# Kernel tuning notes

Measured on AMD Instinct MI355X. Metric: run time of the kernel, lower is better.

The kernel has to match this reference:

```python
import math
import jax, jax.numpy as jnp
import numpy as np

# ---- module constants (from init_kwargs) ----
B, IN, OUT, NR = 4096, 512, 512, 16
WL_MIN, WL_MAX = 1546.0e-9, 1554.0e-9
WL0 = 0.5 * (WL_MIN + WL_MAX)          # center wavelength
R_UM, NEFF, NG = 30.0, 2.34, 4.2
LOSS_DB_CM, KAPPA = 3.0, 0.2
L = 2.0 * math.pi * (R_UM * 1e-6)      # ring circumference [m]
A_AMP = 10.0 ** (-LOSS_DB_CM * (L * 100.0) / 20.0)  # single-pass amplitude
R_T = math.sqrt(1.0 - KAPPA)           # through-coupling amplitude


def _ring_neffs():
    # per-ring effective index detuning from phase_offsets (as in __init__)
    offsets = jnp.linspace(-math.pi, math.pi, NR, dtype=jnp.float32)
    return jnp.float32(NEFF) + offsets * jnp.float32(WL0 / (2.0 * math.pi * L))  # [NR]


def _evaluate_basis(x):
    # wavelengths driven by (clamped) inputs: [B, IN]
    wl = WL_MIN + 0.5 * (jnp.clip(x, -1.0, 1.0) + 1.0) * (WL_MAX - WL_MIN)
    wl = wl[..., None]                                  # [B, IN, 1]
    neff_r = _ring_neffs()                              # [NR]
    # first-order dispersion around WL0 (waveguide with neff, ng)
    neff_wl = neff_r - (wl - WL0) * (NG - neff_r) / WL0  # [B, IN, NR]
    phi = (2.0 * math.pi * L) * neff_wl / wl            # round-trip phase
    c = jnp.cos(phi)
    # all-pass ring power throughput (analytic transfer function)
    num = A_AMP * A_AMP - 2.0 * R_T * A_AMP * c + R_T * R_T
    den = 1.0 - 2.0 * R_T * A_AMP * c + (R_T * A_AMP) ** 2
    return num / den                                    # [B, IN, NR]


def setup_inputs() -> dict:
    key = jax.random.key(0)
    k1, k2, k3 = jax.random.split(key, 3)
    x = jax.random.normal(k1, (B, IN), dtype=jnp.float32)
    coeffs = jax.random.normal(k2, (IN, OUT, NR), dtype=jnp.float32) * 0.05
    base_weight = jax.random.normal(k3, (IN, OUT), dtype=jnp.float32) * 0.05
    return {"x": x, "coeffs": coeffs, "base_weight": base_weight}


def reference(x, coeffs, base_weight):
    basis = _evaluate_basis(x)                          # [B, IN, NR]
    basis_out = jnp.einsum('bin,ion->bo', basis, coeffs)  # [B, OUT]
    residual = x @ base_weight                          # [B, OUT]
    kl = jnp.zeros((1,), dtype=x.dtype)                 # non-variational path
    return (basis_out + residual, kl)
```

## Files before the change

### kernel.cpp

```cpp
#include <hip/hip_runtime.h>
#include <hip/hip_bf16.h>
#include <cmath>
#include <cstdint>

#define Bsz   4096
#define INsz  512
#define OUTsz 512
#define NRING 16
#define KTOT  8704
#define SPLITK 8
#define NPH   17

using short8 = __attribute__((ext_vector_type(8))) short;
using f32x4  = __attribute__((ext_vector_type(4))) float;

struct RC {
  float Cr[NRING];
  float Snr[NRING];
  float K2, SQ, pad0, pad1;
};

__device__ __forceinline__ unsigned short f2bf(float f) {
  __hip_bfloat16 h = __float2bfloat16(f);
  return *reinterpret_cast<unsigned short*>(&h);
}
__device__ __forceinline__ float bf2f(unsigned short u) {
  union { unsigned int u; float f; } v; v.u = (unsigned int)u << 16;
  return v.f;
}
__device__ __forceinline__ float fastrcp(float x) {
#if __has_builtin(__builtin_amdgcn_rcpf)
  return __builtin_amdgcn_rcpf(x);
#else
  return 1.0f / x;
#endif
}
__device__ __forceinline__ float fastfract(float x) {
#if __has_builtin(__builtin_amdgcn_fractf)
  return __builtin_amdgcn_fractf(x);
#else
  return x - floorf(x);
#endif
}
__device__ __forceinline__ float cos2pi(float fr) {
#if __has_builtin(__builtin_amdgcn_cosf)
  return __builtin_amdgcn_cosf(fr);
#else
  return __cosf(fr * 6.28318530717958647692f);
#endif
}
__device__ __forceinline__ float sin2pi(float fr) {
#if __has_builtin(__builtin_amdgcn_sinf)
  return __builtin_amdgcn_sinf(fr);
#else
  return __sinf(fr * 6.28318530717958647692f);
#endif
}

__device__ __forceinline__ void gl_lds16(const void* g, void* l) {
  __builtin_amdgcn_global_load_lds(
      (const __attribute__((address_space(1))) void*)g,
      (__attribute__((address_space(3))) void*)l, 16, 0, 0);
}

__global__ __launch_bounds__(512) void pack_b_kernel(
    const float* __restrict__ coeffs, const float* __restrict__ bw,
    unsigned short* __restrict__ Bt, float* __restrict__ bias, float PQ) {
  __shared__ float red[8];
  const int o = blockIdx.x;
  const int i = threadIdx.x;
  const float* cp = coeffs + ((size_t)i * OUTsz + o) * NRING;
  unsigned short* row = Bt + (size_t)o * KTOT + i;
  float s = 0.0f;
#pragma unroll
  for (int j = 0; j < 4; ++j) {
    f32x4 v = *reinterpret_cast<const f32x4*>(cp + j * 4);
#pragma unroll
    for (int e = 0; e < 4; ++e) {
      const int n = j * 4 + e;
      s += v[e];
      row[(size_t)n * INsz] = f2bf(PQ * v[e]);
    }
  }
  row[(size_t)NRING * INsz] = f2bf(bw[(size_t)i * OUTsz + o]);
#pragma unroll
  for (int off = 32; off > 0; off >>= 1) s += __shfl_down(s, off);
  const int w = i >> 6;
  if ((i & 63) == 0) red[w] = s;
  __syncthreads();
  if (i == 0) {
    float t = 0.0f;
#pragma unroll
    for (int k = 0; k < 8; ++k) t += red[k];
    bias[o] = t;
  }
}

__global__ __launch_bounds__(512, 4) void gemm_fused_kernel(
    const float* __restrict__ x, const unsigned short* __restrict__ Bt,
    unsigned short* __restrict__ part, RC rc) {
  extern __shared__ char smem[];
  char* smA = smem;
  char* smB = smem + 32768;
  const int tid  = threadIdx.x;
  const int lane = tid & 63;
  const int w    = tid >> 6;
  const int bid  = blockIdx.x;
  const int combo = bid & 31;
  const int rb   = bid >> 5;
  const int cb   = combo & 3, ks = combo >> 2;
  const int brow = rb * 128, bcol = cb * 128;

  const int r  = tid & 127;
  const int q4 = tid >> 7;
  const int wb0 = r * 128 + (((q4 * 2 + 0) ^ (r & 7)) * 16);
  const int wb1 = r * 128 + (((q4 * 2 + 1) ^ (r & 7)) * 16);

  const int cg = (lane & 7) ^ ((lane >> 3) & 7);
  const unsigned short* gb0 = Bt + (size_t)(bcol + w * 8 + (lane >> 3)) * KTOT
                                 + ks * 64 + cg * 8;

  const int wr = w >> 2, wc = w & 3;
  const int l7 = lane & 7;
  const int rowA = wr * 64 + (lane & 15);
  const int rowB = wc * 32 + (lane & 15);

  float cth[16], sth[16];
  short8 xbfa, xbfb;
  {
    float xf[16];
    const float* gx = x + (size_t)(brow + r) * INsz + ks * 64 + q4 * 16;
#pragma unroll
    for (int j = 0; j < 4; ++j) {
      f32x4 v = *reinterpret_cast<const f32x4*>(gx + j * 4);
#pragma unroll
      for (int e = 0; e < 4; ++e) xf[j * 4 + e] = v[e];
    }
#pragma unroll
    for (int c = 0; c < 8; ++c) {
      xbfa[c] = (short)f2bf(xf[c]);
      xbfb[c] = (short)f2bf(xf[c + 8]);
    }
#pragma unroll
    for (int c = 0; c < 16; ++c) {
      float xc = fminf(fmaxf(xf[c], -1.0f), 1.0f);
      float wl = __builtin_fmaf(xc, 4.0e-9f, 1550.0e-9f);
      float hh = rc.K2 * xc * fastrcp(wl);
      float fr = fastfract(hh);
      cth[c] = cos2pi(fr);
      sth[c] = sin2pi(fr);
    }
  }

  auto STAGE = [&](int p) {
    char* ldst = smB + (p % 3) * 16384 + w * 1024;
    const unsigned short* src = gb0 + (size_t)p * 512;
    gl_lds16(src, ldst);
    gl_lds16(src + (size_t)64 * KTOT, ldst + 8192);
  };
  auto GENA = [&](int p) {
    char* dst = smA + (p & 1) * 16384;
    if (p < NRING) {
      const float Crn = rc.Cr[p], Snn = rc.Snr[p];
#pragma unroll
      for (int g = 0; g < 2; ++g) {
        short8 wv;
#pragma unroll
        for (int e = 0; e < 8; ++e) {
          float cph = __builtin_fmaf(cth[g * 8 + e], Crn, sth[g * 8 + e] * Snn);
          wv[e] = (short)f2bf(fastrcp(cph + rc.SQ));
        }
        *reinterpret_cast<short8*>(dst + (g ? wb1 : wb0)) = wv;
      }
    } else {
      *reinterpret_cast<short8*>(dst + wb0) = xbfa;
      *reinterpret_cast<short8*>(dst + wb1) = xbfb;
    }
  };

  f32x4 acc[4][2];
#pragma unroll
  for (int m = 0; m < 4; ++m)
#pragma unroll
    for (int q = 0; q < 2; ++q) acc[m][q] = (f32x4){0.f, 0.f, 0.f, 0.f};

  STAGE(0); STAGE(1);
  GENA(0);
  asm volatile("s_waitcnt vmcnt(2) lgkmcnt(0)" ::: "memory");
  __builtin_amdgcn_s_barrier();
  __builtin_amdgcn_sched_barrier(0);

#pragma unroll
  for (int p = 0; p < NPH; ++p) {
    if (p + 2 < NPH) STAGE(p + 2);
    if (p + 1 < NPH) GENA(p + 1);
    const char* bA = smA + (p & 1) * 16384;
    const char* bB = smB + (p % 3) * 16384;
#pragma unroll
    for (int kk = 0; kk < 2; ++kk) {
      const int oct = (((lane >> 4) + kk * 4) ^ l7) * 16;
      short8 af[4], bfr[2];
#pragma unroll
      for (int m = 0; m < 4; ++m)
        af[m] = *reinterpret_cast<const short8*>(bA + (rowA + m * 16) * 128 + oct);
#pragma unroll
      for (int q = 0; q < 2; ++q)
        bfr[q] = *reinterpret_cast<const short8*>(bB + (rowB + q * 16) * 128 + oct);
      __builtin_amdgcn_s_setprio(1);
#pragma unroll
      for (int m = 0; m < 4; ++m)
#pragma unroll
        for (int q = 0; q < 2; ++q)
          acc[m][q] = __builtin_amdgcn_mfma_f32_16x16x32_bf16(af[m], bfr[q], acc[m][q], 0, 0, 0);
      __builtin_amdgcn_s_setprio(0);
    }
    if (p + 1 < NPH) {
      if (p + 2 < NPH) {
        asm volatile("s_waitcnt vmcnt(2) lgkmcnt(0)" ::: "memory");
      } else {
        asm volatile("s_waitcnt vmcnt(0) lgkmcnt(0)" ::: "memory");
      }
      __builtin_amdgcn_s_barrier();
      __builtin_amdgcn_sched_barrier(0);
    }
  }

  unsigned short* po = part + (size_t)ks * ((size_t)Bsz * OUTsz);
  const int r0 = brow + wr * 64 + ((lane >> 4) * 4);
  const int c0 = bcol + wc * 32 + (lane & 15);
#pragma unroll
  for (int m = 0; m < 4; ++m)
#pragma unroll
    for (int q = 0; q < 2; ++q)
#pragma unroll
      for (int e = 0; e < 4; ++e)
        po[(size_t)(r0 + m * 16 + e) * OUTsz + (c0 + q * 16)] = f2bf(acc[m][q][e]);
}

__global__ __launch_bounds__(256) void reduce_kernel(
    const unsigned short* __restrict__ part, const float* __restrict__ bias,
    float* __restrict__ out) {
  const size_t idx  = (size_t)blockIdx.x * 256 + threadIdx.x;
  const size_t base = idx * 8;
  float s[8];
#pragma unroll
  for (int e = 0; e < 8; ++e) s[e] = 0.0f;
#pragma unroll
  for (int sp = 0; sp < SPLITK; ++sp) {
    short8 v = *reinterpret_cast<const short8*>(part + sp * ((size_t)Bsz * OUTsz) + base);
#pragma unroll
    for (int e = 0; e < 8; ++e) s[e] += bf2f((unsigned short)v[e]);
  }
  const int ob = (int)(base & (OUTsz - 1));
  f32x4 b0 = *reinterpret_cast<const f32x4*>(bias + ob);
  f32x4 b1 = *reinterpret_cast<const f32x4*>(bias + ob + 4);
  f32x4 o0 = { s[0] + b0[0], s[1] + b0[1], s[2] + b0[2], s[3] + b0[3] };
  f32x4 o1 = { s[4] + b1[0], s[5] + b1[1], s[6] + b1[2], s[7] + b1[3] };
  *reinterpret_cast<f32x4*>(out + base) = o0;
  *reinterpret_cast<f32x4*>(out + base + 4) = o1;
  if (idx == 0) out[(size_t)Bsz * OUTsz] = 0.0f;
}

extern "C" void kernel_launch(void* const* d_in, const int* in_sizes, int n_in,
                              void* d_out, int out_size, void* d_ws, size_t ws_size,
                              hipStream_t stream) {
  const float* x      = (const float*)d_in[0];
  const float* coeffs = (const float*)d_in[1];
  const float* bw     = (const float*)d_in[2];
  float* out = (float*)d_out;

  unsigned short* Bt   = (unsigned short*)d_ws;
  unsigned short* part = (unsigned short*)((char*)d_ws + (size_t)OUTsz * KTOT * 2);
  float* bias = (float*)((char*)d_ws + (size_t)OUTsz * KTOT * 2
                                     + (size_t)SPLITK * Bsz * OUTsz * 2);

  RC rc;
  float PQ;
  {
    const double PI  = 3.14159265358979323846;
    const double Lc  = 2.0 * PI * 30.0e-6;
    const double WL0 = 1550.0e-9;
    const double NG  = 4.2;
    const double Aamp = pow(10.0, -3.0 * (Lc * 100.0) / 20.0);
    const double Rt2  = 0.8;
    const double Rt   = sqrt(Rt2);
    for (int rr = 0; rr < NRING; ++rr) {
      double off  = -PI + rr * (2.0 * PI / 15.0);
      double neff = 2.34 + off * WL0 / (2.0 * PI * Lc);
      double rev0 = (Lc / WL0) * neff;
      rc.Cr[rr]  = (float)cos(2.0 * PI * rev0);
      rc.Snr[rr] = (float)(-sin(2.0 * PI * rev0));
    }
    const double qn = -2.0 * Rt * Aamp;
    const double s  = 1.0 + Rt2 * Aamp * Aamp;
    const double P  = -(1.0 - Aamp * Aamp) * (1.0 - Rt2);
    rc.K2 = (float)(-4.0e-9 * Lc * NG / WL0);
    rc.SQ = (float)(s / qn);
    rc.pad0 = rc.pad1 = 0.f;
    PQ = (float)(P / qn);
  }

  hipFuncSetAttribute(reinterpret_cast<const void*>(gemm_fused_kernel),
                      hipFuncAttributeMaxDynamicSharedMemorySize, 81920);

  hipLaunchKernelGGL(pack_b_kernel, dim3(OUTsz), dim3(512), 0, stream,
                     coeffs, bw, Bt, bias, PQ);
  hipLaunchKernelGGL(gemm_fused_kernel, dim3(1024), dim3(512), 81920, stream,
                     x, Bt, part, rc);
  hipLaunchKernelGGL(reduce_kernel, dim3((Bsz * OUTsz / 8) / 256), dim3(256), 0, stream,
                     part, bias, out);
}
```

Before: 68.88 us.

## Enlarge GEMM tiles to 256x256, single-buffer A, compute ring phase via fract+cos

Each block now computes a 256x256 output tile instead of 128x128, cutting the grid from 1024 to 256 blocks and raising per-wave MFMA work (8x4 accumulators). The goal is more operand reuse per LDS load and less global B traffic. The A basis tile is now single-buffered. It is regenerated between two barriers each phase, after the second half's fragments are already in registers. The ring phase is now computed as a per-ring fractional offset added to the input phase, followed by one cos, instead of a cos/sin rotation. This drops the sin evaluation and the precomputed sin/cos arrays. The trade-offs are lower occupancy, one block per CU with higher register pressure, and less latency hiding for the basis generation.

```diff
diff --git a/kernel.cpp b/kernel.cpp
--- a/kernel.cpp
+++ b/kernel.cpp
@@ -15,8 +15,7 @@
 using f32x4  = __attribute__((ext_vector_type(4))) float;
 
 struct RC {
-  float Cr[NRING];
-  float Snr[NRING];
+  float Fr[NRING];
   float K2, SQ, pad0, pad1;
 };
 
@@ -47,13 +46,6 @@
   return __builtin_amdgcn_cosf(fr);
 #else
   return __cosf(fr * 6.28318530717958647692f);
-#endif
-}
-__device__ __forceinline__ float sin2pi(float fr) {
-#if __has_builtin(__builtin_amdgcn_sinf)
-  return __builtin_amdgcn_sinf(fr);
-#else
-  return __sinf(fr * 6.28318530717958647692f);
 #endif
 }
 
@@ -96,7 +88,7 @@
   }
 }
 
-__global__ __launch_bounds__(512, 4) void gemm_fused_kernel(
+__global__ __launch_bounds__(512, 2) void gemm_fused_kernel(
     const float* __restrict__ x, const unsigned short* __restrict__ Bt,
     unsigned short* __restrict__ part, RC rc) {
   extern __shared__ char smem[];
@@ -106,15 +98,18 @@
   const int lane = tid & 63;
   const int w    = tid >> 6;
   const int bid  = blockIdx.x;
-  const int combo = bid & 31;
-  const int rb   = bid >> 5;
-  const int cb   = combo & 3, ks = combo >> 2;
-  const int brow = rb * 128, bcol = cb * 128;
-
-  const int r  = tid & 127;
-  const int q4 = tid >> 7;
-  const int wb0 = r * 128 + (((q4 * 2 + 0) ^ (r & 7)) * 16);
-  const int wb1 = r * 128 + (((q4 * 2 + 1) ^ (r & 7)) * 16);
+  const int combo = bid & 15;
+  const int rb   = bid >> 4;
+  const int cb   = combo & 1, ks = combo >> 1;
+  const int brow = rb * 256, bcol = cb * 256;
+
+  const int r  = tid & 255;
+  const int h  = tid >> 8;
+  int wb[4];
+#pragma unroll
+  for (int g = 0; g < 4; ++g)
+    wb[g] = r * 128 + (((h * 4 + g) ^ (r & 7)) * 16);
+  const float* gx = x + (size_t)(brow + r) * INsz + ks * 64 + h * 32;
 
   const int cg = (lane & 7) ^ ((lane >> 3) & 7);
   const unsigned short* gb0 = Bt + (size_t)(bcol + w * 8 + (lane >> 3)) * KTOT
@@ -122,101 +117,110 @@
 
   const int wr = w >> 2, wc = w & 3;
   const int l7 = lane & 7;
-  const int rowA = wr * 64 + (lane & 15);
-  const int rowB = wc * 32 + (lane & 15);
-
-  float cth[16], sth[16];
-  short8 xbfa, xbfb;
-  {
-    float xf[16];
-    const float* gx = x + (size_t)(brow + r) * INsz + ks * 64 + q4 * 16;
-#pragma unroll
-    for (int j = 0; j < 4; ++j) {
-      f32x4 v = *reinterpret_cast<const f32x4*>(gx + j * 4);
-#pragma unroll
-      for (int e = 0; e < 4; ++e) xf[j * 4 + e] = v[e];
-    }
-#pragma unroll
-    for (int c = 0; c < 8; ++c) {
-      xbfa[c] = (short)f2bf(xf[c]);
-      xbfb[c] = (short)f2bf(xf[c + 8]);
-    }
-#pragma unroll
-    for (int c = 0; c < 16; ++c) {
-      float xc = fminf(fmaxf(xf[c], -1.0f), 1.0f);
+  const int rowA = wr * 128 + (lane & 15);
+  const int rowB = wc * 64 + (lane & 15);
+  const int oct0 = (((lane >> 4) + 0) ^ l7) * 16;
+  const int oct1 = (((lane >> 4) + 4) ^ l7) * 16;
+
+  float hrev[32];
+#pragma unroll
+  for (int j = 0; j < 8; ++j) {
+    f32x4 v = *reinterpret_cast<const f32x4*>(gx + j * 4);
+#pragma unroll
+    for (int e = 0; e < 4; ++e) {
+      float xc = fminf(fmaxf(v[e], -1.0f), 1.0f);
       float wl = __builtin_fmaf(xc, 4.0e-9f, 1550.0e-9f);
-      float hh = rc.K2 * xc * fastrcp(wl);
-      float fr = fastfract(hh);
-      cth[c] = cos2pi(fr);
-      sth[c] = sin2pi(fr);
+      hrev[j * 4 + e] = rc.K2 * xc * fastrcp(wl);
     }
   }
 
   auto STAGE = [&](int p) {
-    char* ldst = smB + (p % 3) * 16384 + w * 1024;
+    char* ldst = smB + (p % 3) * 32768 + w * 1024;
     const unsigned short* src = gb0 + (size_t)p * 512;
-    gl_lds16(src, ldst);
-    gl_lds16(src + (size_t)64 * KTOT, ldst + 8192);
+#pragma unroll
+    for (int iss = 0; iss < 4; ++iss)
+      gl_lds16(src + (size_t)iss * 64 * KTOT, ldst + iss * 8192);
   };
-  auto GENA = [&](int p) {
-    char* dst = smA + (p & 1) * 16384;
-    if (p < NRING) {
-      const float Crn = rc.Cr[p], Snn = rc.Snr[p];
-#pragma unroll
-      for (int g = 0; g < 2; ++g) {
+  auto GENA = [&](int ring) {
+    if (ring < NRING) {
+      const float Frn = rc.Fr[ring];
+#pragma unroll
+      for (int g = 0; g < 4; ++g) {
         short8 wv;
 #pragma unroll
         for (int e = 0; e < 8; ++e) {
-          float cph = __builtin_fmaf(cth[g * 8 + e], Crn, sth[g * 8 + e] * Snn);
+          float t = fastfract(hrev[g * 8 + e] + Frn);
+          float cph = cos2pi(t);
           wv[e] = (short)f2bf(fastrcp(cph + rc.SQ));
         }
-        *reinterpret_cast<short8*>(dst + (g ? wb1 : wb0)) = wv;
+        *reinterpret_cast<short8*>(smA + wb[g]) = wv;
       }
     } else {
-      *reinterpret_cast<short8*>(dst + wb0) = xbfa;
-      *reinterpret_cast<short8*>(dst + wb1) = xbfb;
+#pragma unroll
+      for (int g = 0; g < 4; ++g) {
+        f32x4 v0 = *reinterpret_cast<const f32x4*>(gx + g * 8);
+        f32x4 v1 = *reinterpret_cast<const f32x4*>(gx + g * 8 + 4);
+        short8 wv;
+#pragma unroll
+        for (int e = 0; e < 4; ++e) {
+          wv[e]     = (short)f2bf(v0[e]);
+          wv[4 + e] = (short)f2bf(v1[e]);
+        }
+        *reinterpret_cast<short8*>(smA + wb[g]) = wv;
+      }
     }
   };
 
-  f32x4 acc[4][2];
-#pragma unroll
-  for (int m = 0; m < 4; ++m)
-#pragma unroll
-    for (int q = 0; q < 2; ++q) acc[m][q] = (f32x4){0.f, 0.f, 0.f, 0.f};
+  f32x4 acc[8][4];
+#pragma unroll
+  for (int m = 0; m < 8; ++m)
+#pragma unroll
+    for (int q = 0; q < 4; ++q) acc[m][q] = (f32x4){0.f, 0.f, 0.f, 0.f};
 
   STAGE(0); STAGE(1);
   GENA(0);
-  asm volatile("s_waitcnt vmcnt(2) lgkmcnt(0)" ::: "memory");
+  asm volatile("s_waitcnt vmcnt(4) lgkmcnt(0)" ::: "memory");
   __builtin_amdgcn_s_barrier();
   __builtin_amdgcn_sched_barrier(0);
 
 #pragma unroll
   for (int p = 0; p < NPH; ++p) {
+    const char* bB = smB + (p % 3) * 32768;
+    short8 af[8], bv[4];
+#pragma unroll
+    for (int m = 0; m < 8; ++m)
+      af[m] = *reinterpret_cast<const short8*>(smA + (rowA + m * 16) * 128 + oct0);
+#pragma unroll
+    for (int q = 0; q < 4; ++q)
+      bv[q] = *reinterpret_cast<const short8*>(bB + (rowB + q * 16) * 128 + oct0);
     if (p + 2 < NPH) STAGE(p + 2);
+    __builtin_amdgcn_s_setprio(1);
+#pragma unroll
+    for (int m = 0; m < 8; ++m)
+#pragma unroll
+      for (int q = 0; q < 4; ++q)
+        acc[m][q] = __builtin_amdgcn_mfma_f32_16x16x32_bf16(af[m], bv[q], acc[m][q], 0, 0, 0);
+    __builtin_amdgcn_s_setprio(0);
+#pragma unroll
+    for (int m = 0; m < 8; ++m)
+      af[m] = *reinterpret_cast<const short8*>(smA + (rowA + m * 16) * 128 + oct1);
+#pragma unroll
+    for (int q = 0; q < 4; ++q)
+      bv[q] = *reinterpret_cast<const short8*>(bB + (rowB + q * 16) * 128 + oct1);
+    asm volatile("s_waitcnt lgkmcnt(0)" ::: "memory");
+    __builtin_amdgcn_sched_barrier(0);
+    __builtin_amdgcn_s_barrier();
     if (p + 1 < NPH) GENA(p + 1);
-    const char* bA = smA + (p & 1) * 16384;
-    const char* bB = smB + (p % 3) * 16384;
-#pragma unroll
-    for (int kk = 0; kk < 2; ++kk) {
-      const int oct = (((lane >> 4) + kk * 4) ^ l7) * 16;
-      short8 af[4], bfr[2];
-#pragma unroll
-      for (int m = 0; m < 4; ++m)
-        af[m] = *reinterpret_cast<const short8*>(bA + (rowA + m * 16) * 128 + oct);
-#pragma unroll
-      for (int q = 0; q < 2; ++q)
-        bfr[q] = *reinterpret_cast<const short8*>(bB + (rowB + q * 16) * 128 + oct);
-      __builtin_amdgcn_s_setprio(1);
-#pragma unroll
-      for (int m = 0; m < 4; ++m)
-#pragma unroll
-        for (int q = 0; q < 2; ++q)
-          acc[m][q] = __builtin_amdgcn_mfma_f32_16x16x32_bf16(af[m], bfr[q], acc[m][q], 0, 0, 0);
-      __builtin_amdgcn_s_setprio(0);
-    }
+    __builtin_amdgcn_s_setprio(1);
+#pragma unroll
+    for (int m = 0; m < 8; ++m)
+#pragma unroll
+      for (int q = 0; q < 4; ++q)
+        acc[m][q] = __builtin_amdgcn_mfma_f32_16x16x32_bf16(af[m], bv[q], acc[m][q], 0, 0, 0);
+    __builtin_amdgcn_s_setprio(0);
     if (p + 1 < NPH) {
       if (p + 2 < NPH) {
-        asm volatile("s_waitcnt vmcnt(2) lgkmcnt(0)" ::: "memory");
+        asm volatile("s_waitcnt vmcnt(4) lgkmcnt(0)" ::: "memory");
       } else {
         asm volatile("s_waitcnt vmcnt(0) lgkmcnt(0)" ::: "memory");
       }
@@ -226,12 +230,12 @@
   }
 
   unsigned short* po = part + (size_t)ks * ((size_t)Bsz * OUTsz);
-  const int r0 = brow + wr * 64 + ((lane >> 4) * 4);
-  const int c0 = bcol + wc * 32 + (lane & 15);
-#pragma unroll
-  for (int m = 0; m < 4; ++m)
-#pragma unroll
-    for (int q = 0; q < 2; ++q)
+  const int r0 = brow + wr * 128 + ((lane >> 4) * 4);
+  const int c0 = bcol + wc * 64 + (lane & 15);
+#pragma unroll
+  for (int m = 0; m < 8; ++m)
+#pragma unroll
+    for (int q = 0; q < 4; ++q)
 #pragma unroll
       for (int e = 0; e < 4; ++e)
         po[(size_t)(r0 + m * 16 + e) * OUTsz + (c0 + q * 16)] = f2bf(acc[m][q][e]);
@@ -288,8 +292,7 @@
       double off  = -PI + rr * (2.0 * PI / 15.0);
       double neff = 2.34 + off * WL0 / (2.0 * PI * Lc);
       double rev0 = (Lc / WL0) * neff;
-      rc.Cr[rr]  = (float)cos(2.0 * PI * rev0);
-      rc.Snr[rr] = (float)(-sin(2.0 * PI * rev0));
+      rc.Fr[rr] = (float)(rev0 - floor(rev0));
     }
     const double qn = -2.0 * Rt * Aamp;
     const double s  = 1.0 + Rt2 * Aamp * Aamp;
@@ -301,11 +304,11 @@
   }
 
   hipFuncSetAttribute(reinterpret_cast<const void*>(gemm_fused_kernel),
-                      hipFuncAttributeMaxDynamicSharedMemorySize, 81920);
+                      hipFuncAttributeMaxDynamicSharedMemorySize, 131072);
 
   hipLaunchKernelGGL(pack_b_kernel, dim3(OUTsz), dim3(512), 0, stream,
                      coeffs, bw, Bt, bias, PQ);
-  hipLaunchKernelGGL(gemm_fused_kernel, dim3(1024), dim3(512), 81920, stream,
+  hipLaunchKernelGGL(gemm_fused_kernel, dim3(256), dim3(512), 131072, stream,
                      x, Bt, part, rc);
   hipLaunchKernelGGL(reduce_kernel, dim3((Bsz * OUTsz / 8) / 256), dim3(256), 0, stream,
                      part, bias, out);
```

After: 86.52 us. 1.26x slower.

## Widen GEMM tile to 128x256, halve split-K, switch to 32x32 MFMA

Applied to the files above, without the earlier changes.

The fused GEMM now uses 128x256 output tiles, split-K of 4 instead of 8 (34 phases per block), and 32x32x16 bf16 MFMA instructions with all fragment loads hoisted ahead of A-generation. This is meant to raise arithmetic intensity, reduce the bf16 partial-sum traffic into the reduce kernel, and cut redundant basis generation across column tiles. In exchange only 256 blocks launch, which lowers occupancy and parallelism on the device, and LDS use grows to 128 KB per block.

```diff
diff --git a/kernel.cpp b/kernel.cpp
--- a/kernel.cpp
+++ b/kernel.cpp
@@ -8,11 +8,12 @@
 #define OUTsz 512
 #define NRING 16
 #define KTOT  8704
-#define SPLITK 8
-#define NPH   17
+#define SPLITK 4
+#define NPH   34
 
 using short8 = __attribute__((ext_vector_type(8))) short;
 using f32x4  = __attribute__((ext_vector_type(4))) float;
+using f32x16 = __attribute__((ext_vector_type(16))) float;
 
 struct RC {
   float Cr[NRING];
@@ -96,7 +97,7 @@
   }
 }
 
-__global__ __launch_bounds__(512, 4) void gemm_fused_kernel(
+__global__ __launch_bounds__(512) void gemm_fused_kernel(
     const float* __restrict__ x, const unsigned short* __restrict__ Bt,
     unsigned short* __restrict__ part, RC rc) {
   extern __shared__ char smem[];
@@ -106,10 +107,10 @@
   const int lane = tid & 63;
   const int w    = tid >> 6;
   const int bid  = blockIdx.x;
-  const int combo = bid & 31;
-  const int rb   = bid >> 5;
-  const int cb   = combo & 3, ks = combo >> 2;
-  const int brow = rb * 128, bcol = cb * 128;
+  const int combo = bid & 7;
+  const int rb   = bid >> 3;
+  const int cb   = combo & 1, ks = combo >> 1;
+  const int brow = rb * 128, bcol = cb * 256;
 
   const int r  = tid & 127;
   const int q4 = tid >> 7;
@@ -117,30 +118,30 @@
   const int wb1 = r * 128 + (((q4 * 2 + 1) ^ (r & 7)) * 16);
 
   const int cg = (lane & 7) ^ ((lane >> 3) & 7);
-  const unsigned short* gb0 = Bt + (size_t)(bcol + w * 8 + (lane >> 3)) * KTOT
-                                 + ks * 64 + cg * 8;
+  const unsigned short* gb0 = Bt + (size_t)(bcol + w * 8 + (lane >> 3)) * KTOT + cg * 8;
 
   const int wr = w >> 2, wc = w & 3;
   const int l7 = lane & 7;
-  const int rowA = wr * 64 + (lane & 15);
-  const int rowB = wc * 32 + (lane & 15);
-
-  float cth[16], sth[16];
-  short8 xbfa, xbfb;
-  {
-    float xf[16];
-    const float* gx = x + (size_t)(brow + r) * INsz + ks * 64 + q4 * 16;
-#pragma unroll
-    for (int j = 0; j < 4; ++j) {
-      f32x4 v = *reinterpret_cast<const f32x4*>(gx + j * 4);
-#pragma unroll
-      for (int e = 0; e < 4; ++e) xf[j * 4 + e] = v[e];
-    }
-#pragma unroll
-    for (int c = 0; c < 8; ++c) {
-      xbfa[c] = (short)f2bf(xf[c]);
-      xbfb[c] = (short)f2bf(xf[c + 8]);
-    }
+  const int l5 = lane >> 5;
+  const int rowA = wr * 64 + (lane & 31);
+  const int rowB = wc * 64 + (lane & 31);
+
+  float xf0[16], xf1[16], cth[16], sth[16];
+  short8 xbf0a, xbf0b, xbf1a, xbf1b;
+  const float* gx = x + (size_t)(brow + r) * INsz + ks * 128 + q4 * 16;
+#pragma unroll
+  for (int j = 0; j < 4; ++j) {
+    f32x4 v0 = *reinterpret_cast<const f32x4*>(gx + j * 4);
+    f32x4 v1 = *reinterpret_cast<const f32x4*>(gx + 64 + j * 4);
+#pragma unroll
+    for (int e = 0; e < 4; ++e) { xf0[j * 4 + e] = v0[e]; xf1[j * 4 + e] = v1[e]; }
+  }
+#pragma unroll
+  for (int c = 0; c < 8; ++c) {
+    xbf0a[c] = (short)f2bf(xf0[c]);     xbf0b[c] = (short)f2bf(xf0[c + 8]);
+    xbf1a[c] = (short)f2bf(xf1[c]);     xbf1b[c] = (short)f2bf(xf1[c + 8]);
+  }
+  auto TRIG = [&](const float* xf) {
 #pragma unroll
     for (int c = 0; c < 16; ++c) {
       float xc = fminf(fmaxf(xf[c], -1.0f), 1.0f);
@@ -150,18 +151,23 @@
       cth[c] = cos2pi(fr);
       sth[c] = sin2pi(fr);
     }
-  }
+  };
+  TRIG(xf0);
 
   auto STAGE = [&](int p) {
-    char* ldst = smB + (p % 3) * 16384 + w * 1024;
-    const unsigned short* src = gb0 + (size_t)p * 512;
-    gl_lds16(src, ldst);
-    gl_lds16(src + (size_t)64 * KTOT, ldst + 8192);
+    const int is = (p >= 17) ? 1 : 0, n = p - 17 * is;
+    const size_t koff = (size_t)(n * 512 + ks * 128 + is * 64);
+    char* ldst = smB + (p % 3) * 32768 + w * 1024;
+    const unsigned short* src = gb0 + koff;
+#pragma unroll
+    for (int iss = 0; iss < 4; ++iss)
+      gl_lds16(src + (size_t)iss * 64 * KTOT, ldst + iss * 8192);
   };
   auto GENA = [&](int p) {
+    const int is = (p >= 17) ? 1 : 0, n = p - 17 * is;
     char* dst = smA + (p & 1) * 16384;
-    if (p < NRING) {
-      const float Crn = rc.Cr[p], Snn = rc.Snr[p];
+    if (n < NRING) {
+      const float Crn = rc.Cr[n], Snn = rc.Snr[n];
 #pragma unroll
       for (int g = 0; g < 2; ++g) {
         short8 wv;
@@ -173,50 +179,55 @@
         *reinterpret_cast<short8*>(dst + (g ? wb1 : wb0)) = wv;
       }
     } else {
-      *reinterpret_cast<short8*>(dst + wb0) = xbfa;
-      *reinterpret_cast<short8*>(dst + wb1) = xbfb;
+      *reinterpret_cast<short8*>(dst + wb0) = is ? xbf1a : xbf0a;
+      *reinterpret_cast<short8*>(dst + wb1) = is ? xbf1b : xbf0b;
     }
   };
 
-  f32x4 acc[4][2];
-#pragma unroll
-  for (int m = 0; m < 4; ++m)
-#pragma unroll
-    for (int q = 0; q < 2; ++q) acc[m][q] = (f32x4){0.f, 0.f, 0.f, 0.f};
+  f32x16 acc[2][2];
+#pragma unroll
+  for (int m = 0; m < 2; ++m)
+#pragma unroll
+    for (int q = 0; q < 2; ++q)
+#pragma unroll
+      for (int e = 0; e < 16; ++e) acc[m][q][e] = 0.0f;
 
   STAGE(0); STAGE(1);
   GENA(0);
-  asm volatile("s_waitcnt vmcnt(2) lgkmcnt(0)" ::: "memory");
+  asm volatile("s_waitcnt vmcnt(4) lgkmcnt(0)" ::: "memory");
   __builtin_amdgcn_s_barrier();
   __builtin_amdgcn_sched_barrier(0);
 
 #pragma unroll
   for (int p = 0; p < NPH; ++p) {
     if (p + 2 < NPH) STAGE(p + 2);
+    if (p == 16) TRIG(xf1);
+    const char* bA = smA + (p & 1) * 16384;
+    const char* bB = smB + (p % 3) * 32768;
+    short8 af[4][2], bv[4][2];
+#pragma unroll
+    for (int kk = 0; kk < 4; ++kk) {
+      const int oct = ((kk * 2 + l5) ^ l7) * 16;
+#pragma unroll
+      for (int m = 0; m < 2; ++m)
+        af[kk][m] = *reinterpret_cast<const short8*>(bA + (rowA + m * 32) * 128 + oct);
+#pragma unroll
+      for (int q = 0; q < 2; ++q)
+        bv[kk][q] = *reinterpret_cast<const short8*>(bB + (rowB + q * 32) * 128 + oct);
+    }
     if (p + 1 < NPH) GENA(p + 1);
-    const char* bA = smA + (p & 1) * 16384;
-    const char* bB = smB + (p % 3) * 16384;
-#pragma unroll
-    for (int kk = 0; kk < 2; ++kk) {
-      const int oct = (((lane >> 4) + kk * 4) ^ l7) * 16;
-      short8 af[4], bfr[2];
-#pragma unroll
-      for (int m = 0; m < 4; ++m)
-        af[m] = *reinterpret_cast<const short8*>(bA + (rowA + m * 16) * 128 + oct);
-#pragma unroll
-      for (int q = 0; q < 2; ++q)
-        bfr[q] = *reinterpret_cast<const short8*>(bB + (rowB + q * 16) * 128 + oct);
-      __builtin_amdgcn_s_setprio(1);
-#pragma unroll
-      for (int m = 0; m < 4; ++m)
+    __builtin_amdgcn_s_setprio(1);
+#pragma unroll
+    for (int kk = 0; kk < 4; ++kk)
+#pragma unroll
+      for (int m = 0; m < 2; ++m)
 #pragma unroll
         for (int q = 0; q < 2; ++q)
-          acc[m][q] = __builtin_amdgcn_mfma_f32_16x16x32_bf16(af[m], bfr[q], acc[m][q], 0, 0, 0);
-      __builtin_amdgcn_s_setprio(0);
-    }
+          acc[m][q] = __builtin_amdgcn_mfma_f32_32x32x16_bf16(af[kk][m], bv[kk][q], acc[m][q], 0, 0, 0);
+    __builtin_amdgcn_s_setprio(0);
     if (p + 1 < NPH) {
       if (p + 2 < NPH) {
-        asm volatile("s_waitcnt vmcnt(2) lgkmcnt(0)" ::: "memory");
+        asm volatile("s_waitcnt vmcnt(4) lgkmcnt(0)" ::: "memory");
       } else {
         asm volatile("s_waitcnt vmcnt(0) lgkmcnt(0)" ::: "memory");
       }
@@ -226,15 +237,17 @@
   }
 
   unsigned short* po = part + (size_t)ks * ((size_t)Bsz * OUTsz);
-  const int r0 = brow + wr * 64 + ((lane >> 4) * 4);
-  const int c0 = bcol + wc * 32 + (lane & 15);
-#pragma unroll
-  for (int m = 0; m < 4; ++m)
+  const int r0 = brow + wr * 64 + 4 * l5;
+  const int c0 = bcol + wc * 64 + (lane & 31);
+#pragma unroll
+  for (int m = 0; m < 2; ++m)
 #pragma unroll
     for (int q = 0; q < 2; ++q)
 #pragma unroll
-      for (int e = 0; e < 4; ++e)
-        po[(size_t)(r0 + m * 16 + e) * OUTsz + (c0 + q * 16)] = f2bf(acc[m][q][e]);
+      for (int reg = 0; reg < 16; ++reg) {
+        const int row = r0 + m * 32 + (reg & 3) + 8 * (reg >> 2);
+        po[(size_t)row * OUTsz + (c0 + q * 32)] = f2bf(acc[m][q][reg]);
+      }
 }
 
 __global__ __launch_bounds__(256) void reduce_kernel(
@@ -301,11 +314,11 @@
   }
 
   hipFuncSetAttribute(reinterpret_cast<const void*>(gemm_fused_kernel),
-                      hipFuncAttributeMaxDynamicSharedMemorySize, 81920);
+                      hipFuncAttributeMaxDynamicSharedMemorySize, 131072);
 
   hipLaunchKernelGGL(pack_b_kernel, dim3(OUTsz), dim3(512), 0, stream,
                      coeffs, bw, Bt, bias, PQ);
-  hipLaunchKernelGGL(gemm_fused_kernel, dim3(1024), dim3(512), 81920, stream,
+  hipLaunchKernelGGL(gemm_fused_kernel, dim3(256), dim3(512), 131072, stream,
                      x, Bt, part, rc);
   hipLaunchKernelGGL(reduce_kernel, dim3((Bsz * OUTsz / 8) / 256), dim3(256), 0, stream,
                      part, bias, out);
```

Measured after the change: 64.65 us. -6.1%, faster.
